# Optimization experiments

Hardware: AMD Instinct MI355X
Metric: run time of the kernel (lower is better)

Reference implementation:

```python
import math
import jax, jax.numpy as jnp
import numpy as np

C_COEF = 3  # module attribute c


def setup_inputs() -> dict:
    key = jax.random.key(0)
    k1, k2, k3 = jax.random.split(key, 3)
    B, L, D = 16, 4096, 64
    return {
        "Q": jax.random.normal(k1, (B, L, D), jnp.float32),
        "K": jax.random.normal(k2, (B, L, D), jnp.float32),
        "V": jax.random.normal(k3, (B, L, D), jnp.float32),
    }


def _fit_len(x, L):
    # K.at[:, 0:L, :].get(mode='fill', fill_value=0): truncate or zero-pad to length L
    S = x.shape[1]
    if S >= L:
        return x[:, :L]
    return jnp.pad(x, ((0, 0), (0, L - S), (0, 0)))


def reference(Q, K, V):
    B, L, D = Q.shape
    K = _fit_len(K, L)
    V = _fit_len(V, L)

    # FFT-based circular cross-correlation Rxx[b, tau, d]
    Qf = jnp.fft.rfft(Q, axis=1)
    Kf = jnpp_rfft = jnp.fft.rfft(K, axis=1)
    Rxx = jnp.fft.irfft(Qf * jnp.conjugate(Kf), n=L, axis=1)  # [B, L, D]

    k = min(int(math.floor(C_COEF * math.log(L))), L)
    # top-k delays per (batch, channel)
    Wk, Ik = jax.lax.top_k(jnp.moveaxis(Rxx, 1, -1), k)  # [B, D, k]
    Wk = jax.nn.softmax(Wk, axis=-1)

    # roll(v, -i)[l] == v[(l + i) % L]  -> single fused gather over all (B, D, k)
    idx = (jnp.arange(L)[None, None, None, :] + Ik[..., None]) % L  # [B, D, k, L]
    Vt = jnp.moveaxis(V, 1, -1)  # [B, D, L]
    Vg = jnp.take_along_axis(Vt[:, :, None, :], idx, axis=3)  # [B, D, k, L]

    # softmax-weighted accumulation over the k delays
    A = jnp.einsum('bdk,bdkl->bld', Wk, Vg)  # [B, L, D]
    return A
```

## Files before the change

kernel.cpp:

```cpp
#include <hip/hip_runtime.h>


#define FFT_N 4096
#define TOPK  24
#define PI2   6.28318530717958647692f
#define C16_1 0.92387953251128675613f
#define S16_1 0.38268343236508977173f
#define C16_2 0.70710678118654752440f

#define V1OFF   4608
#define SM_CAND 36864
#define SM_C0   37376
#define SM_PACK 38400
#define SM_CNT  38608
#define SM_THR  38612
#define SM_SIZE 38624

__device__ __forceinline__ float2 cmul(float2 a, float2 b) {
  return make_float2(a.x*b.x - a.y*b.y, a.x*b.y + a.y*b.x);
}

__device__ __forceinline__ unsigned fkey(float f) {
  int b = __float_as_int(f);
  return (unsigned)(b ^ ((b >> 31) | 0x80000000));
}

template<int S>
__device__ __forceinline__ void fft16(float2* x) {
  const float sg = (float)S;
  float2 y[16];
#pragma unroll
  for (int n2 = 0; n2 < 4; ++n2) {
    float2 a = x[n2], b = x[4+n2], c = x[8+n2], d = x[12+n2];
    float t0r=a.x+c.x, t0i=a.y+c.y, t1r=a.x-c.x, t1i=a.y-c.y;
    float t2r=b.x+d.x, t2i=b.y+d.y, t3r=b.x-d.x, t3i=b.y-d.y;
    y[n2*4+0] = make_float2(t0r+t2r, t0i+t2i);
    y[n2*4+2] = make_float2(t0r-t2r, t0i-t2i);
    y[n2*4+1] = make_float2(t1r - sg*t3i, t1i + sg*t3r);
    y[n2*4+3] = make_float2(t1r + sg*t3i, t1i - sg*t3r);
  }
#define CTW(ii, cc, ss) { float2 v=y[ii]; y[ii]=make_float2(v.x*(cc)-v.y*(sg*(ss)), v.x*(sg*(ss))+v.y*(cc)); }
  CTW(5,  C16_1, S16_1)
  CTW(6,  C16_2, C16_2)
  CTW(7,  S16_1, C16_1)
  CTW(9,  C16_2, C16_2)
  { float2 v = y[10]; y[10] = make_float2(-sg*v.y, sg*v.x); }
  CTW(11, -C16_2, C16_2)
  CTW(13, S16_1, C16_1)
  CTW(14, -C16_2, C16_2)
  CTW(15, -C16_1, -S16_1)
#undef CTW
#pragma unroll
  for (int k1 = 0; k1 < 4; ++k1) {
    float2 a = y[k1], b = y[4+k1], c = y[8+k1], d = y[12+k1];
    float t0r=a.x+c.x, t0i=a.y+c.y, t1r=a.x-c.x, t1i=a.y-c.y;
    float t2r=b.x+d.x, t2i=b.y+d.y, t3r=b.x-d.x, t3i=b.y-d.y;
    x[k1+0]  = make_float2(t0r+t2r, t0i+t2i);
    x[k1+8]  = make_float2(t0r-t2r, t0i-t2i);
    x[k1+4]  = make_float2(t1r - sg*t3i, t1i + sg*t3r);
    x[k1+12] = make_float2(t1r + sg*t3i, t1i - sg*t3r);
  }
}

__device__ __forceinline__ void twiddle_chain(float2* x, float ang) {
  float sb, cb; __sincosf(ang, &sb, &cb);
  float2 w1 = make_float2(cb, sb);
  float2 w2 = cmul(w1,w1), w3 = cmul(w1,w2);
  float2 w4 = cmul(w2,w2), w5 = cmul(w2,w3), w6 = cmul(w3,w3), w7 = cmul(w3,w4);
  float2 w8 = cmul(w4,w4), w9 = cmul(w4,w5), w10 = cmul(w5,w5), w11 = cmul(w5,w6);
  float2 w12 = cmul(w6,w6), w13 = cmul(w6,w7), w14 = cmul(w7,w7), w15 = cmul(w7,w8);
  x[1]=cmul(x[1],w1);   x[2]=cmul(x[2],w2);   x[3]=cmul(x[3],w3);
  x[4]=cmul(x[4],w4);   x[5]=cmul(x[5],w5);   x[6]=cmul(x[6],w6);
  x[7]=cmul(x[7],w7);   x[8]=cmul(x[8],w8);   x[9]=cmul(x[9],w9);
  x[10]=cmul(x[10],w10); x[11]=cmul(x[11],w11); x[12]=cmul(x[12],w12);
  x[13]=cmul(x[13],w13); x[14]=cmul(x[14],w14); x[15]=cmul(x[15],w15);
}

__global__ __launch_bounds__(256) void transposeQKV(const float* __restrict__ Q,
                                                    const float* __restrict__ K,
                                                    const float* __restrict__ V,
                                                    float2* __restrict__ ZQK,
                                                    float* __restrict__ Vt) {
  __shared__ float tq[64][65];
  __shared__ float tk[64][65];
  __shared__ float tv[64][65];
  const int b = blockIdx.y;
  const int t0 = blockIdx.x << 6;
  const float* Qb = Q + ((size_t)b << 18);
  const float* Kb = K + ((size_t)b << 18);
  const float* Vb = V + ((size_t)b << 18);
  int tx = threadIdx.x & 63, ty = threadIdx.x >> 6;
#pragma unroll
  for (int i = 0; i < 16; ++i) {
    int r = (i << 2) + ty;
    tq[r][tx] = Qb[(size_t)(t0 + r) * 64 + tx];
    tk[r][tx] = Kb[(size_t)(t0 + r) * 64 + tx];
    tv[r][tx] = Vb[(size_t)(t0 + r) * 64 + tx];
  }
  __syncthreads();
  float2* zoutb = ZQK + ((size_t)b << 18);
  float*  voutb = Vt + ((size_t)b << 18);
#pragma unroll
  for (int i = 0; i < 16; ++i) {
    int d = (i << 2) + ty;
    zoutb[(size_t)d * 4096 + t0 + tx] = make_float2(tq[tx][d], tk[tx][d]);
    voutb[(size_t)d * 4096 + t0 + tx] = tv[tx][d];
  }
}

__global__ __launch_bounds__(256) void transpose64(const float* __restrict__ in,
                                                   float* __restrict__ out,
                                                   int R, int C) {
  __shared__ float tile[64][65];
  int tiles_c = C >> 6;
  int tr = blockIdx.x / tiles_c;
  int tc = blockIdx.x - tr * tiles_c;
  const float* inb = in + (size_t)blockIdx.y * R * C;
  float* outb = out + (size_t)blockIdx.y * R * C;
  int tx = threadIdx.x & 63;
  int ty = threadIdx.x >> 6;
  int r0 = tr << 6, c0 = tc << 6;
#pragma unroll
  for (int i = 0; i < 16; ++i) {
    int r = (i << 2) + ty;
    tile[r][tx] = inb[(size_t)(r0 + r) * C + (c0 + tx)];
  }
  __syncthreads();
#pragma unroll
  for (int i = 0; i < 16; ++i) {
    int r = (i << 2) + ty;
    outb[(size_t)(c0 + r) * R + (r0 + tx)] = tile[tx][r];
  }
}

__global__ __launch_bounds__(256, 4) void corr_kernel(const float2* __restrict__ ZQK,
                                                      const float* __restrict__ Vt,
                                                      float* __restrict__ At) {
  __shared__ __align__(16) unsigned char smem[SM_SIZE];
  float2* Z = (float2*)smem;

  const int tid = threadIdx.x;
  const size_t row = (size_t)blockIdx.x << 12;

  float2 x[16];

#pragma unroll
  for (int n1 = 0; n1 < 16; ++n1)
    x[n1] = ZQK[row + (n1 << 8) + tid];
  fft16<-1>(x);
  twiddle_chain(x, -PI2 * (float)tid / 4096.f);
#pragma unroll
  for (int k = 0; k < 16; ++k) Z[(k << 8) + tid] = x[k];
  __syncthreads();
  {
    const int k1 = tid >> 4, b = tid & 15;
#pragma unroll
    for (int a = 0; a < 16; ++a) x[a] = Z[(k1 << 8) + (a << 4) + b];
    fft16<-1>(x);
    twiddle_chain(x, -PI2 * (float)b / 256.f);
    __syncthreads();
#pragma unroll
    for (int cc = 0; cc < 16; ++cc) Z[(k1 << 8) + (cc << 4) + (b ^ cc)] = x[cc];
  }
  __syncthreads();
  {
    const int k1 = tid >> 4, c = tid & 15;
#pragma unroll
    for (int bb = 0; bb < 16; ++bb) x[bb] = Z[(k1 << 8) + (c << 4) + (bb ^ c)];
    fft16<-1>(x);
    __syncthreads();
    const int bf = k1 + (c << 4);
#pragma unroll
    for (int d = 0; d < 16; ++d) Z[(bf ^ c) + (d << 8)] = x[d];
  }
  __syncthreads();

  {
    const float scale = 0.25f / 4096.f;
    const int x1 = tid >> 4;
#pragma unroll
    for (int f1 = 0; f1 < 16; ++f1) {
      int f  = (f1 << 8) + tid;
      int fp = (4096 - f) & 4095;
      float2 A  = Z[f ^ x1];
      float2 Bv = Z[fp ^ ((fp >> 4) & 15)];
      float ur = A.x + Bv.x, ui = A.y - Bv.y;
      float vr = A.x - Bv.x, vi = -A.y - Bv.y;
      float xr = ur*vr - ui*vi, xi = ur*vi + ui*vr;
      x[f1] = make_float2(-xi * scale, xr * scale);
    }
  }

  float4 v4s[4];
#pragma unroll
  for (int mm = 0; mm < 4; ++mm)
    v4s[mm] = *(const float4*)&Vt[row + (tid << 2) + (mm << 10)];

  fft16<1>(x);
  twiddle_chain(x, PI2 * (float)tid / 4096.f);
  __syncthreads();
#pragma unroll
  for (int k = 0; k < 16; ++k) Z[(k << 8) + tid] = x[k];
  __syncthreads();
  {
    const int k1 = tid >> 4, b = tid & 15;
#pragma unroll
    for (int a = 0; a < 16; ++a) x[a] = Z[(k1 << 8) + (a << 4) + b];
    fft16<1>(x);
    twiddle_chain(x, PI2 * (float)b / 256.f);
    __syncthreads();
#pragma unroll
    for (int cc = 0; cc < 16; ++cc) Z[(k1 << 8) + (cc << 4) + (b ^ cc)] = x[cc];
  }
  __syncthreads();
  float rr[16];
  {
    const int k1 = tid >> 4, c = tid & 15;
#pragma unroll
    for (int bb = 0; bb < 16; ++bb) x[bb] = Z[(k1 << 8) + (c << 4) + (bb ^ c)];
    fft16<1>(x);
#pragma unroll
    for (int d = 0; d < 16; ++d) rr[d] = x[d].x;
  }
  __syncthreads();

  float* Vf = (float*)smem;
#pragma unroll
  for (int mm = 0; mm < 4; ++mm) {
    int n0 = (tid << 2) + (mm << 10);
    float4 v = v4s[mm];
    *(float4*)&Vf[n0] = v;
    Vf[V1OFF + ((n0 - 1) & 4095)] = v.x;
    Vf[V1OFF + n0]     = v.y;
    Vf[V1OFF + n0 + 1] = v.z;
    Vf[V1OFF + n0 + 2] = v.w;
  }
  {
    float4 v = v4s[0];
    if (tid < 128) {
      *(float4*)&Vf[4096 + (tid << 2)] = v;
      Vf[V1OFF + 4096 + (tid << 2) + 0] = v.y;
      Vf[V1OFF + 4096 + (tid << 2) + 1] = v.z;
      Vf[V1OFF + 4096 + (tid << 2) + 2] = v.w;
    }
    if (tid >= 1 && tid <= 128)
      Vf[V1OFF + 4096 + (tid << 2) - 1] = v.x;
  }
  float c0v = rr[0];
#pragma unroll
  for (int d = 1; d < 16; ++d) c0v = fmaxf(c0v, rr[d]);
  ((float*)(smem + SM_C0))[tid] = c0v;
  if (tid == 0) *(int*)(smem + SM_CNT) = 0;
  __syncthreads();

  if (tid < 64) {
    const float* c0b = (const float*)(smem + SM_C0);
    unsigned k0 = fkey(c0b[tid]);
    unsigned k1 = fkey(c0b[tid + 64]);
    unsigned k2 = fkey(c0b[tid + 128]);
    unsigned k3 = fkey(c0b[tid + 192]);
    unsigned T = 0;
    for (int b = 31; b >= 16; --b) {
      unsigned T2 = T | (1u << b);
      int c = (k0 >= T2) + (k1 >= T2) + (k2 >= T2) + (k3 >= T2);
      unsigned long long b0 = __ballot(c & 1);
      unsigned long long b1 = __ballot(c & 2);
      unsigned long long b2 = __ballot(c & 4);
      int cnt = __popcll(b0) + 2 * __popcll(b1) + 4 * __popcll(b2);
      if (cnt >= TOPK) T = T2;
    }
    if (tid == 0) {
      float thrF;
      if (T == 0) thrF = -3e38f;
      else {
        int ib = (T & 0x80000000u) ? (int)(T ^ 0x80000000u) : (int)~T;
        thrF = __int_as_float(ib);
      }
      *(float*)(smem + SM_THR) = thrF;
    }
  }
  __syncthreads();

  {
    const float thrF = *(const float*)(smem + SM_THR);
    int* cnt = (int*)(smem + SM_CNT);
    float2* cand = (float2*)(smem + SM_CAND);
    const int tb = (tid >> 4) + ((tid & 15) << 4);
#pragma unroll
    for (int d = 0; d < 16; ++d) {
      if (rr[d] >= thrF) {
        int pos = atomicAdd(cnt, 1);
        if (pos < 64)
          cand[pos] = make_float2(rr[d], __int_as_float(tb + (d << 8)));
      }
    }
  }
  __syncthreads();

  if (tid < 64) {
    const float2* cand = (const float2*)(smem + SM_CAND);
    int NC = *(const int*)(smem + SM_CNT);
    NC = NC < 64 ? NC : 64;
    float v; int ix;
    if (tid < NC) { float2 cc = cand[tid]; v = cc.x; ix = __float_as_int(cc.y); }
    else          { v = -3e38f; ix = 0x7fffffff; }
#pragma unroll
    for (int k = 2; k <= 64; k <<= 1) {
#pragma unroll
      for (int j = k >> 1; j > 0; j >>= 1) {
        float ov = __shfl_xor(v, j);
        int   oi = __shfl_xor(ix, j);
        bool iless  = (tid & j) == 0;
        bool dird   = (tid & k) == 0;
        bool better = (v > ov) || (v == ov && ix < oi);
        bool keep   = ((iless == dird) == better);
        v  = keep ? v  : ov;
        ix = keep ? ix : oi;
      }
    }
    float m0 = __shfl(v, 0);
    float e = (tid < TOPK) ? __expf(v - m0) : 0.f;
    float es = e;
#pragma unroll
    for (int off = 32; off; off >>= 1) es += __shfl_xor(es, off);
    float2* pack = (float2*)(smem + SM_PACK);
    if (tid < TOPK) pack[tid] = make_float2(e, __int_as_float(ix));
    if (tid == 0)   pack[TOPK] = make_float2(es, 0.f);
  }
  __syncthreads();

  const float2* pack = (const float2*)(smem + SM_PACK);
  const float inv = 1.0f / pack[TOPK].x;
  float2 a0 = make_float2(0,0), a1=a0, a2=a0, a3=a0, a4=a0, a5=a0, a6=a0, a7=a0;
  const int lbase = tid << 1;
#pragma unroll 1
  for (int t = 0; t < TOPK; ++t) {
    float2 p_ = pack[t];
    float e  = p_.x;
    int   ik = __float_as_int(p_.y);
    int base = ik & ~1;
    const float* Vb = Vf + ((ik & 1) ? V1OFF : 0);
    int e0 = (lbase        + base) & 4095;
    int e1 = (lbase + 1024 + base) & 4095;
    int e2 = (lbase + 2048 + base) & 4095;
    int e3 = (lbase + 3072 + base) & 4095;
    float2 v00 = *(const float2*)&Vb[e0];
    float2 v01 = *(const float2*)&Vb[e0 + 512];
    float2 v10 = *(const float2*)&Vb[e1];
    float2 v11 = *(const float2*)&Vb[e1 + 512];
    float2 v20 = *(const float2*)&Vb[e2];
    float2 v21 = *(const float2*)&Vb[e2 + 512];
    float2 v30 = *(const float2*)&Vb[e3];
    float2 v31 = *(const float2*)&Vb[e3 + 512];
    a0.x += e*v00.x; a0.y += e*v00.y;
    a1.x += e*v01.x; a1.y += e*v01.y;
    a2.x += e*v10.x; a2.y += e*v10.y;
    a3.x += e*v11.x; a3.y += e*v11.y;
    a4.x += e*v20.x; a4.y += e*v20.y;
    a5.x += e*v21.x; a5.y += e*v21.y;
    a6.x += e*v30.x; a6.y += e*v30.y;
    a7.x += e*v31.x; a7.y += e*v31.y;
  }
  *(float2*)&At[row + lbase]        = make_float2(a0.x*inv, a0.y*inv);
  *(float2*)&At[row + lbase + 512]  = make_float2(a1.x*inv, a1.y*inv);
  *(float2*)&At[row + lbase + 1024] = make_float2(a2.x*inv, a2.y*inv);
  *(float2*)&At[row + lbase + 1536] = make_float2(a3.x*inv, a3.y*inv);
  *(float2*)&At[row + lbase + 2048] = make_float2(a4.x*inv, a4.y*inv);
  *(float2*)&At[row + lbase + 2560] = make_float2(a5.x*inv, a5.y*inv);
  *(float2*)&At[row + lbase + 3072] = make_float2(a6.x*inv, a6.y*inv);
  *(float2*)&At[row + lbase + 3584] = make_float2(a7.x*inv, a7.y*inv);
}

extern "C" void kernel_launch(void* const* d_in, const int* in_sizes, int n_in,
                              void* d_out, int out_size, void* d_ws, size_t ws_size,
                              hipStream_t stream) {
  const float* Q = (const float*)d_in[0];
  const float* K = (const float*)d_in[1];
  const float* V = (const float*)d_in[2];
  float* out = (float*)d_out;
  float* wsf = (float*)d_ws;

  const int B = 16;
  const size_t SLAB = (size_t)4194304;
  float2* ZQK = (float2*)wsf;
  float*  Vt  = wsf + 2 * SLAB;
  float*  At  = Vt;

  dim3 blk(256);
  transposeQKV<<<dim3(64, B), blk, 0, stream>>>(Q, K, V, ZQK, Vt);
  corr_kernel<<<dim3(B * 64), blk, 0, stream>>>(ZQK, Vt, At);
  transpose64<<<dim3(64, B), blk, 0, stream>>>(At, out, 64, 4096);
}
```

Baseline: 55.11 us.

## Restructure FFT as radix-8 four-pass with 512 threads per block

Replaces the three-pass radix-16 FFT (256 threads, 16 elements each) with a four-pass radix-8 FFT using 512 threads holding 8 elements each. Padded shared-memory strides (RK1/RK2) are used instead of XOR swizzles in the intermediate passes. The top-k threshold search and the gather/accumulate are adapted to 512 threads, and the output is now written as contiguous float4 chunks. The aim is lower register pressure and more parallelism per block, at the cost of an extra FFT pass and its barriers.

```diff
diff --git a/kernel.cpp b/kernel.cpp
--- a/kernel.cpp
+++ b/kernel.cpp
@@ -1,20 +1,19 @@
 #include <hip/hip_runtime.h>
 
 
-#define FFT_N 4096
 #define TOPK  24
 #define PI2   6.28318530717958647692f
-#define C16_1 0.92387953251128675613f
-#define S16_1 0.38268343236508977173f
-#define C16_2 0.70710678118654752440f
+#define SQH   0.70710678118654752440f
 
 #define V1OFF   4608
-#define SM_CAND 36864
-#define SM_C0   37376
-#define SM_PACK 38400
-#define SM_CNT  38608
-#define SM_THR  38612
-#define SM_SIZE 38624
+#define SM_C0   36864
+#define SM_CAND 38912
+#define SM_PACK 39424
+#define SM_CNT  39624
+#define SM_THR  39628
+#define SM_SIZE 39632
+#define RK1     528
+#define RK2     66
 
 __device__ __forceinline__ float2 cmul(float2 a, float2 b) {
   return make_float2(a.x*b.x - a.y*b.y, a.x*b.y + a.y*b.x);
@@ -25,55 +24,44 @@
   return (unsigned)(b ^ ((b >> 31) | 0x80000000));
 }
 
+__device__ __forceinline__ int SPw(int q) { return q ^ ((q >> 4) & 15); }
+
 template<int S>
-__device__ __forceinline__ void fft16(float2* x) {
+__device__ __forceinline__ void fft8(float2* x) {
   const float sg = (float)S;
-  float2 y[16];
-#pragma unroll
-  for (int n2 = 0; n2 < 4; ++n2) {
-    float2 a = x[n2], b = x[4+n2], c = x[8+n2], d = x[12+n2];
-    float t0r=a.x+c.x, t0i=a.y+c.y, t1r=a.x-c.x, t1i=a.y-c.y;
-    float t2r=b.x+d.x, t2i=b.y+d.y, t3r=b.x-d.x, t3i=b.y-d.y;
-    y[n2*4+0] = make_float2(t0r+t2r, t0i+t2i);
-    y[n2*4+2] = make_float2(t0r-t2r, t0i-t2i);
-    y[n2*4+1] = make_float2(t1r - sg*t3i, t1i + sg*t3r);
-    y[n2*4+3] = make_float2(t1r + sg*t3i, t1i - sg*t3r);
-  }
-#define CTW(ii, cc, ss) { float2 v=y[ii]; y[ii]=make_float2(v.x*(cc)-v.y*(sg*(ss)), v.x*(sg*(ss))+v.y*(cc)); }
-  CTW(5,  C16_1, S16_1)
-  CTW(6,  C16_2, C16_2)
-  CTW(7,  S16_1, C16_1)
-  CTW(9,  C16_2, C16_2)
-  { float2 v = y[10]; y[10] = make_float2(-sg*v.y, sg*v.x); }
-  CTW(11, -C16_2, C16_2)
-  CTW(13, S16_1, C16_1)
-  CTW(14, -C16_2, C16_2)
-  CTW(15, -C16_1, -S16_1)
-#undef CTW
-#pragma unroll
-  for (int k1 = 0; k1 < 4; ++k1) {
-    float2 a = y[k1], b = y[4+k1], c = y[8+k1], d = y[12+k1];
-    float t0r=a.x+c.x, t0i=a.y+c.y, t1r=a.x-c.x, t1i=a.y-c.y;
-    float t2r=b.x+d.x, t2i=b.y+d.y, t3r=b.x-d.x, t3i=b.y-d.y;
-    x[k1+0]  = make_float2(t0r+t2r, t0i+t2i);
-    x[k1+8]  = make_float2(t0r-t2r, t0i-t2i);
-    x[k1+4]  = make_float2(t1r - sg*t3i, t1i + sg*t3r);
-    x[k1+12] = make_float2(t1r + sg*t3i, t1i - sg*t3r);
-  }
-}
-
-__device__ __forceinline__ void twiddle_chain(float2* x, float ang) {
+  float et0r=x[0].x+x[4].x, et0i=x[0].y+x[4].y;
+  float et1r=x[0].x-x[4].x, et1i=x[0].y-x[4].y;
+  float et2r=x[2].x+x[6].x, et2i=x[2].y+x[6].y;
+  float et3r=x[2].x-x[6].x, et3i=x[2].y-x[6].y;
+  float E0r=et0r+et2r, E0i=et0i+et2i;
+  float E2r=et0r-et2r, E2i=et0i-et2i;
+  float E1r=et1r-sg*et3i, E1i=et1i+sg*et3r;
+  float E3r=et1r+sg*et3i, E3i=et1i-sg*et3r;
+  float ot0r=x[1].x+x[5].x, ot0i=x[1].y+x[5].y;
+  float ot1r=x[1].x-x[5].x, ot1i=x[1].y-x[5].y;
+  float ot2r=x[3].x+x[7].x, ot2i=x[3].y+x[7].y;
+  float ot3r=x[3].x-x[7].x, ot3i=x[3].y-x[7].y;
+  float O0r=ot0r+ot2r, O0i=ot0i+ot2i;
+  float O2r=ot0r-ot2r, O2i=ot0i-ot2i;
+  float O1r=ot1r-sg*ot3i, O1i=ot1i+sg*ot3r;
+  float O3r=ot1r+sg*ot3i, O3i=ot1i-sg*ot3r;
+  float T1r = SQH*(O1r - sg*O1i), T1i = SQH*(O1i + sg*O1r);
+  float T2r = -sg*O2i,            T2i = sg*O2r;
+  float T3r = -SQH*(O3r + sg*O3i), T3i = SQH*(sg*O3r - O3i);
+  x[0]=make_float2(E0r+O0r, E0i+O0i);  x[4]=make_float2(E0r-O0r, E0i-O0i);
+  x[1]=make_float2(E1r+T1r, E1i+T1i);  x[5]=make_float2(E1r-T1r, E1i-T1i);
+  x[2]=make_float2(E2r+T2r, E2i+T2i);  x[6]=make_float2(E2r-T2r, E2i-T2i);
+  x[3]=make_float2(E3r+T3r, E3i+T3i);  x[7]=make_float2(E3r-T3r, E3i-T3i);
+}
+
+__device__ __forceinline__ void twiddle8(float2* x, float ang) {
   float sb, cb; __sincosf(ang, &sb, &cb);
   float2 w1 = make_float2(cb, sb);
-  float2 w2 = cmul(w1,w1), w3 = cmul(w1,w2);
-  float2 w4 = cmul(w2,w2), w5 = cmul(w2,w3), w6 = cmul(w3,w3), w7 = cmul(w3,w4);
-  float2 w8 = cmul(w4,w4), w9 = cmul(w4,w5), w10 = cmul(w5,w5), w11 = cmul(w5,w6);
-  float2 w12 = cmul(w6,w6), w13 = cmul(w6,w7), w14 = cmul(w7,w7), w15 = cmul(w7,w8);
-  x[1]=cmul(x[1],w1);   x[2]=cmul(x[2],w2);   x[3]=cmul(x[3],w3);
-  x[4]=cmul(x[4],w4);   x[5]=cmul(x[5],w5);   x[6]=cmul(x[6],w6);
-  x[7]=cmul(x[7],w7);   x[8]=cmul(x[8],w8);   x[9]=cmul(x[9],w9);
-  x[10]=cmul(x[10],w10); x[11]=cmul(x[11],w11); x[12]=cmul(x[12],w12);
-  x[13]=cmul(x[13],w13); x[14]=cmul(x[14],w14); x[15]=cmul(x[15],w15);
+  float2 w2 = cmul(w1,w1), w3 = cmul(w2,w1);
+  float2 w4 = cmul(w2,w2), w5 = cmul(w3,w2), w6 = cmul(w3,w3), w7 = cmul(w4,w3);
+  x[1]=cmul(x[1],w1); x[2]=cmul(x[2],w2); x[3]=cmul(x[3],w3);
+  x[4]=cmul(x[4],w4); x[5]=cmul(x[5],w5); x[6]=cmul(x[6],w6);
+  x[7]=cmul(x[7],w7);
 }
 
 __global__ __launch_bounds__(256) void transposeQKV(const float* __restrict__ Q,
@@ -133,101 +121,133 @@
   }
 }
 
-__global__ __launch_bounds__(256, 4) void corr_kernel(const float2* __restrict__ ZQK,
+__global__ __launch_bounds__(512, 8) void corr_kernel(const float2* __restrict__ ZQK,
                                                       const float* __restrict__ Vt,
                                                       float* __restrict__ At) {
   __shared__ __align__(16) unsigned char smem[SM_SIZE];
   float2* Z = (float2*)smem;
 
   const int tid = threadIdx.x;
+  const int k1 = tid >> 6;
   const size_t row = (size_t)blockIdx.x << 12;
 
-  float2 x[16];
-
-#pragma unroll
-  for (int n1 = 0; n1 < 16; ++n1)
-    x[n1] = ZQK[row + (n1 << 8) + tid];
-  fft16<-1>(x);
-  twiddle_chain(x, -PI2 * (float)tid / 4096.f);
-#pragma unroll
-  for (int k = 0; k < 16; ++k) Z[(k << 8) + tid] = x[k];
-  __syncthreads();
-  {
-    const int k1 = tid >> 4, b = tid & 15;
-#pragma unroll
-    for (int a = 0; a < 16; ++a) x[a] = Z[(k1 << 8) + (a << 4) + b];
-    fft16<-1>(x);
-    twiddle_chain(x, -PI2 * (float)b / 256.f);
-    __syncthreads();
-#pragma unroll
-    for (int cc = 0; cc < 16; ++cc) Z[(k1 << 8) + (cc << 4) + (b ^ cc)] = x[cc];
-  }
-  __syncthreads();
-  {
-    const int k1 = tid >> 4, c = tid & 15;
-#pragma unroll
-    for (int bb = 0; bb < 16; ++bb) x[bb] = Z[(k1 << 8) + (c << 4) + (bb ^ c)];
-    fft16<-1>(x);
-    __syncthreads();
-    const int bf = k1 + (c << 4);
-#pragma unroll
-    for (int d = 0; d < 16; ++d) Z[(bf ^ c) + (d << 8)] = x[d];
+  float2 x[8];
+
+#pragma unroll
+  for (int j = 0; j < 8; ++j)
+    x[j] = ZQK[row + (j << 9) + tid];
+  fft8<-1>(x);
+  twiddle8(x, -PI2 * (float)tid / 4096.f);
+#pragma unroll
+  for (int k = 0; k < 8; ++k) Z[k * RK1 + tid] = x[k];
+  __syncthreads();
+
+  {
+    const int u = tid & 63;
+    float2* Zb = Z + k1 * RK1;
+#pragma unroll
+    for (int a = 0; a < 8; ++a) x[a] = Zb[(a << 6) + u];
+    fft8<-1>(x);
+    twiddle8(x, -PI2 * (float)u / 512.f);
+    __syncthreads();
+#pragma unroll
+    for (int k = 0; k < 8; ++k) Zb[k * RK2 + u] = x[k];
+  }
+  __syncthreads();
+
+  {
+    const int k2 = (tid >> 3) & 7, v = tid & 7;
+    float2* Zb = Z + k1 * RK1 + k2 * RK2;
+#pragma unroll
+    for (int b = 0; b < 8; ++b) x[b] = Zb[(b << 3) + v];
+    fft8<-1>(x);
+    twiddle8(x, -PI2 * (float)v / 64.f);
+    __syncthreads();
+#pragma unroll
+    for (int k = 0; k < 8; ++k) Zb[(k << 3) + v] = x[k];
+  }
+  __syncthreads();
+
+  const int flo = k1 + (((tid >> 3) & 7) << 3) + ((tid & 7) << 6);
+  {
+    const int k2 = (tid >> 3) & 7, k3 = tid & 7;
+    const float2* Zb = Z + k1 * RK1 + k2 * RK2 + (k3 << 3);
+#pragma unroll
+    for (int c = 0; c < 8; ++c) x[c] = Zb[c];
+    fft8<-1>(x);
+    __syncthreads();
+#pragma unroll
+    for (int d = 0; d < 8; ++d) Z[SPw(flo + (d << 9))] = x[d];
   }
   __syncthreads();
 
   {
     const float scale = 0.25f / 4096.f;
-    const int x1 = tid >> 4;
-#pragma unroll
-    for (int f1 = 0; f1 < 16; ++f1) {
-      int f  = (f1 << 8) + tid;
+    const int sw_own = (tid >> 4) & 15;
+#pragma unroll
+    for (int j = 0; j < 8; ++j) {
+      int f  = (j << 9) + tid;
       int fp = (4096 - f) & 4095;
-      float2 A  = Z[f ^ x1];
-      float2 Bv = Z[fp ^ ((fp >> 4) & 15)];
+      float2 A  = Z[f ^ sw_own];
+      float2 Bv = Z[SPw(fp)];
       float ur = A.x + Bv.x, ui = A.y - Bv.y;
       float vr = A.x - Bv.x, vi = -A.y - Bv.y;
       float xr = ur*vr - ui*vi, xi = ur*vi + ui*vr;
-      x[f1] = make_float2(-xi * scale, xr * scale);
-    }
-  }
-
-  float4 v4s[4];
-#pragma unroll
-  for (int mm = 0; mm < 4; ++mm)
-    v4s[mm] = *(const float4*)&Vt[row + (tid << 2) + (mm << 10)];
-
-  fft16<1>(x);
-  twiddle_chain(x, PI2 * (float)tid / 4096.f);
-  __syncthreads();
-#pragma unroll
-  for (int k = 0; k < 16; ++k) Z[(k << 8) + tid] = x[k];
-  __syncthreads();
-  {
-    const int k1 = tid >> 4, b = tid & 15;
-#pragma unroll
-    for (int a = 0; a < 16; ++a) x[a] = Z[(k1 << 8) + (a << 4) + b];
-    fft16<1>(x);
-    twiddle_chain(x, PI2 * (float)b / 256.f);
-    __syncthreads();
-#pragma unroll
-    for (int cc = 0; cc < 16; ++cc) Z[(k1 << 8) + (cc << 4) + (b ^ cc)] = x[cc];
-  }
-  __syncthreads();
-  float rr[16];
-  {
-    const int k1 = tid >> 4, c = tid & 15;
-#pragma unroll
-    for (int bb = 0; bb < 16; ++bb) x[bb] = Z[(k1 << 8) + (c << 4) + (bb ^ c)];
-    fft16<1>(x);
-#pragma unroll
-    for (int d = 0; d < 16; ++d) rr[d] = x[d].x;
+      x[j] = make_float2(-xi * scale, xr * scale);
+    }
+  }
+
+  float4 v4s[2];
+#pragma unroll
+  for (int mm = 0; mm < 2; ++mm)
+    v4s[mm] = *(const float4*)&Vt[row + (tid << 2) + (mm << 11)];
+  __syncthreads();
+
+  fft8<1>(x);
+  twiddle8(x, PI2 * (float)tid / 4096.f);
+#pragma unroll
+  for (int k = 0; k < 8; ++k) Z[k * RK1 + tid] = x[k];
+  __syncthreads();
+  {
+    const int u = tid & 63;
+    float2* Zb = Z + k1 * RK1;
+#pragma unroll
+    for (int a = 0; a < 8; ++a) x[a] = Zb[(a << 6) + u];
+    fft8<1>(x);
+    twiddle8(x, PI2 * (float)u / 512.f);
+    __syncthreads();
+#pragma unroll
+    for (int k = 0; k < 8; ++k) Zb[k * RK2 + u] = x[k];
+  }
+  __syncthreads();
+  {
+    const int k2 = (tid >> 3) & 7, v = tid & 7;
+    float2* Zb = Z + k1 * RK1 + k2 * RK2;
+#pragma unroll
+    for (int b = 0; b < 8; ++b) x[b] = Zb[(b << 3) + v];
+    fft8<1>(x);
+    twiddle8(x, PI2 * (float)v / 64.f);
+    __syncthreads();
+#pragma unroll
+    for (int k = 0; k < 8; ++k) Zb[(k << 3) + v] = x[k];
+  }
+  __syncthreads();
+  float rr[8];
+  {
+    const int k2 = (tid >> 3) & 7, k3 = tid & 7;
+    const float2* Zb = Z + k1 * RK1 + k2 * RK2 + (k3 << 3);
+#pragma unroll
+    for (int c = 0; c < 8; ++c) x[c] = Zb[c];
+    fft8<1>(x);
+#pragma unroll
+    for (int d = 0; d < 8; ++d) rr[d] = x[d].x;
   }
   __syncthreads();
 
   float* Vf = (float*)smem;
 #pragma unroll
-  for (int mm = 0; mm < 4; ++mm) {
-    int n0 = (tid << 2) + (mm << 10);
+  for (int mm = 0; mm < 2; ++mm) {
+    int n0 = (tid << 2) + (mm << 11);
     float4 v = v4s[mm];
     *(float4*)&Vf[n0] = v;
     Vf[V1OFF + ((n0 - 1) & 4095)] = v.x;
@@ -248,25 +268,27 @@
   }
   float c0v = rr[0];
 #pragma unroll
-  for (int d = 1; d < 16; ++d) c0v = fmaxf(c0v, rr[d]);
+  for (int d = 1; d < 8; ++d) c0v = fmaxf(c0v, rr[d]);
   ((float*)(smem + SM_C0))[tid] = c0v;
   if (tid == 0) *(int*)(smem + SM_CNT) = 0;
   __syncthreads();
 
   if (tid < 64) {
     const float* c0b = (const float*)(smem + SM_C0);
-    unsigned k0 = fkey(c0b[tid]);
-    unsigned k1 = fkey(c0b[tid + 64]);
-    unsigned k2 = fkey(c0b[tid + 128]);
-    unsigned k3 = fkey(c0b[tid + 192]);
+    unsigned kk[8];
+#pragma unroll
+    for (int m = 0; m < 8; ++m) kk[m] = fkey(c0b[tid + (m << 6)]);
     unsigned T = 0;
     for (int b = 31; b >= 16; --b) {
       unsigned T2 = T | (1u << b);
-      int c = (k0 >= T2) + (k1 >= T2) + (k2 >= T2) + (k3 >= T2);
+      int c = 0;
+#pragma unroll
+      for (int m = 0; m < 8; ++m) c += (kk[m] >= T2) ? 1 : 0;
       unsigned long long b0 = __ballot(c & 1);
       unsigned long long b1 = __ballot(c & 2);
       unsigned long long b2 = __ballot(c & 4);
-      int cnt = __popcll(b0) + 2 * __popcll(b1) + 4 * __popcll(b2);
+      unsigned long long b3 = __ballot(c & 8);
+      int cnt = __popcll(b0) + 2*__popcll(b1) + 4*__popcll(b2) + 8*__popcll(b3);
       if (cnt >= TOPK) T = T2;
     }
     if (tid == 0) {
@@ -285,13 +307,12 @@
     const float thrF = *(const float*)(smem + SM_THR);
     int* cnt = (int*)(smem + SM_CNT);
     float2* cand = (float2*)(smem + SM_CAND);
-    const int tb = (tid >> 4) + ((tid & 15) << 4);
-#pragma unroll
-    for (int d = 0; d < 16; ++d) {
+#pragma unroll
+    for (int d = 0; d < 8; ++d) {
       if (rr[d] >= thrF) {
         int pos = atomicAdd(cnt, 1);
         if (pos < 64)
-          cand[pos] = make_float2(rr[d], __int_as_float(tb + (d << 8)));
+          cand[pos] = make_float2(rr[d], __int_as_float(flo + (d << 9)));
       }
     }
   }
@@ -331,8 +352,8 @@
 
   const float2* pack = (const float2*)(smem + SM_PACK);
   const float inv = 1.0f / pack[TOPK].x;
-  float2 a0 = make_float2(0,0), a1=a0, a2=a0, a3=a0, a4=a0, a5=a0, a6=a0, a7=a0;
-  const int lbase = tid << 1;
+  float2 a0 = make_float2(0,0), a1 = a0, a2 = a0, a3 = a0;
+  const int o = tid << 3;
 #pragma unroll 1
   for (int t = 0; t < TOPK; ++t) {
     float2 p_ = pack[t];
@@ -340,35 +361,20 @@
     int   ik = __float_as_int(p_.y);
     int base = ik & ~1;
     const float* Vb = Vf + ((ik & 1) ? V1OFF : 0);
-    int e0 = (lbase        + base) & 4095;
-    int e1 = (lbase + 1024 + base) & 4095;
-    int e2 = (lbase + 2048 + base) & 4095;
-    int e3 = (lbase + 3072 + base) & 4095;
-    float2 v00 = *(const float2*)&Vb[e0];
-    float2 v01 = *(const float2*)&Vb[e0 + 512];
-    float2 v10 = *(const float2*)&Vb[e1];
-    float2 v11 = *(const float2*)&Vb[e1 + 512];
-    float2 v20 = *(const float2*)&Vb[e2];
-    float2 v21 = *(const float2*)&Vb[e2 + 512];
-    float2 v30 = *(const float2*)&Vb[e3];
-    float2 v31 = *(const float2*)&Vb[e3 + 512];
-    a0.x += e*v00.x; a0.y += e*v00.y;
-    a1.x += e*v01.x; a1.y += e*v01.y;
-    a2.x += e*v10.x; a2.y += e*v10.y;
-    a3.x += e*v11.x; a3.y += e*v11.y;
-    a4.x += e*v20.x; a4.y += e*v20.y;
-    a5.x += e*v21.x; a5.y += e*v21.y;
-    a6.x += e*v30.x; a6.y += e*v30.y;
-    a7.x += e*v31.x; a7.y += e*v31.y;
-  }
-  *(float2*)&At[row + lbase]        = make_float2(a0.x*inv, a0.y*inv);
-  *(float2*)&At[row + lbase + 512]  = make_float2(a1.x*inv, a1.y*inv);
-  *(float2*)&At[row + lbase + 1024] = make_float2(a2.x*inv, a2.y*inv);
-  *(float2*)&At[row + lbase + 1536] = make_float2(a3.x*inv, a3.y*inv);
-  *(float2*)&At[row + lbase + 2048] = make_float2(a4.x*inv, a4.y*inv);
-  *(float2*)&At[row + lbase + 2560] = make_float2(a5.x*inv, a5.y*inv);
-  *(float2*)&At[row + lbase + 3072] = make_float2(a6.x*inv, a6.y*inv);
-  *(float2*)&At[row + lbase + 3584] = make_float2(a7.x*inv, a7.y*inv);
+    int e0 = (o + base) & 4095;
+    float2 v0 = *(const float2*)&Vb[e0];
+    float2 v1 = *(const float2*)&Vb[e0 + 2];
+    float2 v2 = *(const float2*)&Vb[e0 + 4];
+    float2 v3 = *(const float2*)&Vb[e0 + 6];
+    a0.x += e*v0.x; a0.y += e*v0.y;
+    a1.x += e*v1.x; a1.y += e*v1.y;
+    a2.x += e*v2.x; a2.y += e*v2.y;
+    a3.x += e*v3.x; a3.y += e*v3.y;
+  }
+  float4 r0 = make_float4(a0.x*inv, a0.y*inv, a1.x*inv, a1.y*inv);
+  float4 r1 = make_float4(a2.x*inv, a2.y*inv, a3.x*inv, a3.y*inv);
+  *(float4*)&At[row + o]     = r0;
+  *(float4*)&At[row + o + 4] = r1;
 }
 
 extern "C" void kernel_launch(void* const* d_in, const int* in_sizes, int n_in,
@@ -388,6 +394,6 @@
 
   dim3 blk(256);
   transposeQKV<<<dim3(64, B), blk, 0, stream>>>(Q, K, V, ZQK, Vt);
-  corr_kernel<<<dim3(B * 64), blk, 0, stream>>>(ZQK, Vt, At);
+  corr_kernel<<<dim3(B * 64), dim3(512), 0, stream>>>(ZQK, Vt, At);
   transpose64<<<dim3(64, B), blk, 0, stream>>>(At, out, 64, 4096);
 }
```

After: 70.00 us. +27.0%, slower.

## Pad FFT shared rows and drop barriers between warp-local FFT stages

Applied to the files above, without the earlier changes.

Shared-memory rows in the first FFT stage are padded to a stride of 272, so the column-wise reads no longer conflict. The second and third radix-16 stages now exchange data through a 16-thread private region without a block barrier, which removes several __syncthreads calls per FFT. The shifted copy of V is rebuilt with wrap-around indexing instead of extended buffers, which shrinks shared memory use. The risk is that the barrier-free exchange relies on the 16 threads of a group sitting in the same wavefront, and the shifted copy adds an extra barrier plus reads from shared memory.

```diff
diff --git a/kernel.cpp b/kernel.cpp
--- a/kernel.cpp
+++ b/kernel.cpp
@@ -1,20 +1,20 @@
 #include <hip/hip_runtime.h>
 
 
-#define FFT_N 4096
 #define TOPK  24
 #define PI2   6.28318530717958647692f
 #define C16_1 0.92387953251128675613f
 #define S16_1 0.38268343236508977173f
 #define C16_2 0.70710678118654752440f
 
-#define V1OFF   4608
-#define SM_CAND 36864
-#define SM_C0   37376
-#define SM_PACK 38400
-#define SM_CNT  38608
-#define SM_THR  38612
-#define SM_SIZE 38624
+#define RK    272
+#define V1OFF   4096
+#define SM_C0   34816
+#define SM_CAND 35840
+#define SM_PACK 36352
+#define SM_CNT  36552
+#define SM_THR  36556
+#define SM_SIZE 36560
 
 __device__ __forceinline__ float2 cmul(float2 a, float2 b) {
   return make_float2(a.x*b.x - a.y*b.y, a.x*b.y + a.y*b.x);
@@ -140,6 +140,7 @@
   float2* Z = (float2*)smem;
 
   const int tid = threadIdx.x;
+  const int k1 = tid >> 4, bq = tid & 15;
   const size_t row = (size_t)blockIdx.x << 12;
 
   float2 x[16];
@@ -150,39 +151,35 @@
   fft16<-1>(x);
   twiddle_chain(x, -PI2 * (float)tid / 4096.f);
 #pragma unroll
-  for (int k = 0; k < 16; ++k) Z[(k << 8) + tid] = x[k];
-  __syncthreads();
-  {
-    const int k1 = tid >> 4, b = tid & 15;
-#pragma unroll
-    for (int a = 0; a < 16; ++a) x[a] = Z[(k1 << 8) + (a << 4) + b];
+  for (int k = 0; k < 16; ++k) Z[k * RK + tid] = x[k];
+  __syncthreads();
+
+  {
+#pragma unroll
+    for (int a = 0; a < 16; ++a) x[a] = Z[k1 * RK + (a << 4) + bq];
     fft16<-1>(x);
-    twiddle_chain(x, -PI2 * (float)b / 256.f);
-    __syncthreads();
-#pragma unroll
-    for (int cc = 0; cc < 16; ++cc) Z[(k1 << 8) + (cc << 4) + (b ^ cc)] = x[cc];
-  }
-  __syncthreads();
-  {
-    const int k1 = tid >> 4, c = tid & 15;
-#pragma unroll
-    for (int bb = 0; bb < 16; ++bb) x[bb] = Z[(k1 << 8) + (c << 4) + (bb ^ c)];
+    twiddle_chain(x, -PI2 * (float)bq / 256.f);
+#pragma unroll
+    for (int cc = 0; cc < 16; ++cc) Z[k1 * RK + (cc << 4) + (bq ^ cc)] = x[cc];
+#pragma unroll
+    for (int bb = 0; bb < 16; ++bb) x[bb] = Z[k1 * RK + (bq << 4) + (bb ^ bq)];
     fft16<-1>(x);
-    __syncthreads();
-    const int bf = k1 + (c << 4);
-#pragma unroll
-    for (int d = 0; d < 16; ++d) Z[(bf ^ c) + (d << 8)] = x[d];
+  }
+  __syncthreads();
+  {
+    const int bf = k1 + (bq << 4);
+#pragma unroll
+    for (int d = 0; d < 16; ++d) Z[(bf ^ bq) + (d << 8)] = x[d];
   }
   __syncthreads();
 
   {
     const float scale = 0.25f / 4096.f;
-    const int x1 = tid >> 4;
 #pragma unroll
     for (int f1 = 0; f1 < 16; ++f1) {
       int f  = (f1 << 8) + tid;
       int fp = (4096 - f) & 4095;
-      float2 A  = Z[f ^ x1];
+      float2 A  = Z[f ^ k1];
       float2 Bv = Z[fp ^ ((fp >> 4) & 15)];
       float ur = A.x + Bv.x, ui = A.y - Bv.y;
       float vr = A.x - Bv.x, vi = -A.y - Bv.y;
@@ -195,74 +192,58 @@
 #pragma unroll
   for (int mm = 0; mm < 4; ++mm)
     v4s[mm] = *(const float4*)&Vt[row + (tid << 2) + (mm << 10)];
+  __syncthreads();
 
   fft16<1>(x);
   twiddle_chain(x, PI2 * (float)tid / 4096.f);
-  __syncthreads();
-#pragma unroll
-  for (int k = 0; k < 16; ++k) Z[(k << 8) + tid] = x[k];
-  __syncthreads();
-  {
-    const int k1 = tid >> 4, b = tid & 15;
-#pragma unroll
-    for (int a = 0; a < 16; ++a) x[a] = Z[(k1 << 8) + (a << 4) + b];
+#pragma unroll
+  for (int k = 0; k < 16; ++k) Z[k * RK + tid] = x[k];
+  __syncthreads();
+  {
+#pragma unroll
+    for (int a = 0; a < 16; ++a) x[a] = Z[k1 * RK + (a << 4) + bq];
     fft16<1>(x);
-    twiddle_chain(x, PI2 * (float)b / 256.f);
-    __syncthreads();
-#pragma unroll
-    for (int cc = 0; cc < 16; ++cc) Z[(k1 << 8) + (cc << 4) + (b ^ cc)] = x[cc];
-  }
-  __syncthreads();
+    twiddle_chain(x, PI2 * (float)bq / 256.f);
+#pragma unroll
+    for (int cc = 0; cc < 16; ++cc) Z[k1 * RK + (cc << 4) + (bq ^ cc)] = x[cc];
+#pragma unroll
+    for (int bb = 0; bb < 16; ++bb) x[bb] = Z[k1 * RK + (bq << 4) + (bb ^ bq)];
+    fft16<1>(x);
+  }
   float rr[16];
-  {
-    const int k1 = tid >> 4, c = tid & 15;
-#pragma unroll
-    for (int bb = 0; bb < 16; ++bb) x[bb] = Z[(k1 << 8) + (c << 4) + (bb ^ c)];
-    fft16<1>(x);
-#pragma unroll
-    for (int d = 0; d < 16; ++d) rr[d] = x[d].x;
-  }
+#pragma unroll
+  for (int d = 0; d < 16; ++d) rr[d] = x[d].x;
   __syncthreads();
 
   float* Vf = (float*)smem;
+#pragma unroll
+  for (int mm = 0; mm < 4; ++mm)
+    *(float4*)&Vf[(tid << 2) + (mm << 10)] = v4s[mm];
+  float c0v = rr[0];
+#pragma unroll
+  for (int d = 1; d < 16; ++d) c0v = fmaxf(c0v, rr[d]);
+  ((float*)(smem + SM_C0))[tid] = c0v;
+  if (tid == 0) *(int*)(smem + SM_CNT) = 0;
+  __syncthreads();
+
 #pragma unroll
   for (int mm = 0; mm < 4; ++mm) {
     int n0 = (tid << 2) + (mm << 10);
     float4 v = v4s[mm];
-    *(float4*)&Vf[n0] = v;
-    Vf[V1OFF + ((n0 - 1) & 4095)] = v.x;
-    Vf[V1OFF + n0]     = v.y;
-    Vf[V1OFF + n0 + 1] = v.z;
-    Vf[V1OFF + n0 + 2] = v.w;
-  }
-  {
-    float4 v = v4s[0];
-    if (tid < 128) {
-      *(float4*)&Vf[4096 + (tid << 2)] = v;
-      Vf[V1OFF + 4096 + (tid << 2) + 0] = v.y;
-      Vf[V1OFF + 4096 + (tid << 2) + 1] = v.z;
-      Vf[V1OFF + 4096 + (tid << 2) + 2] = v.w;
-    }
-    if (tid >= 1 && tid <= 128)
-      Vf[V1OFF + 4096 + (tid << 2) - 1] = v.x;
-  }
-  float c0v = rr[0];
-#pragma unroll
-  for (int d = 1; d < 16; ++d) c0v = fmaxf(c0v, rr[d]);
-  ((float*)(smem + SM_C0))[tid] = c0v;
-  if (tid == 0) *(int*)(smem + SM_CNT) = 0;
-  __syncthreads();
+    float nx = Vf[(n0 + 4) & 4095];
+    *(float4*)&Vf[V1OFF + n0] = make_float4(v.y, v.z, v.w, nx);
+  }
 
   if (tid < 64) {
     const float* c0b = (const float*)(smem + SM_C0);
-    unsigned k0 = fkey(c0b[tid]);
-    unsigned k1 = fkey(c0b[tid + 64]);
-    unsigned k2 = fkey(c0b[tid + 128]);
-    unsigned k3 = fkey(c0b[tid + 192]);
+    unsigned kk0 = fkey(c0b[tid]);
+    unsigned kk1 = fkey(c0b[tid + 64]);
+    unsigned kk2 = fkey(c0b[tid + 128]);
+    unsigned kk3 = fkey(c0b[tid + 192]);
     unsigned T = 0;
     for (int b = 31; b >= 16; --b) {
       unsigned T2 = T | (1u << b);
-      int c = (k0 >= T2) + (k1 >= T2) + (k2 >= T2) + (k3 >= T2);
+      int c = (kk0 >= T2) + (kk1 >= T2) + (kk2 >= T2) + (kk3 >= T2);
       unsigned long long b0 = __ballot(c & 1);
       unsigned long long b1 = __ballot(c & 2);
       unsigned long long b2 = __ballot(c & 4);
@@ -285,7 +266,7 @@
     const float thrF = *(const float*)(smem + SM_THR);
     int* cnt = (int*)(smem + SM_CNT);
     float2* cand = (float2*)(smem + SM_CAND);
-    const int tb = (tid >> 4) + ((tid & 15) << 4);
+    const int tb = k1 + (bq << 4);
 #pragma unroll
     for (int d = 0; d < 16; ++d) {
       if (rr[d] >= thrF) {
@@ -332,7 +313,7 @@
   const float2* pack = (const float2*)(smem + SM_PACK);
   const float inv = 1.0f / pack[TOPK].x;
   float2 a0 = make_float2(0,0), a1=a0, a2=a0, a3=a0, a4=a0, a5=a0, a6=a0, a7=a0;
-  const int lbase = tid << 1;
+  const int o2 = tid << 1;
 #pragma unroll 1
   for (int t = 0; t < TOPK; ++t) {
     float2 p_ = pack[t];
@@ -340,35 +321,18 @@
     int   ik = __float_as_int(p_.y);
     int base = ik & ~1;
     const float* Vb = Vf + ((ik & 1) ? V1OFF : 0);
-    int e0 = (lbase        + base) & 4095;
-    int e1 = (lbase + 1024 + base) & 4095;
-    int e2 = (lbase + 2048 + base) & 4095;
-    int e3 = (lbase + 3072 + base) & 4095;
-    float2 v00 = *(const float2*)&Vb[e0];
-    float2 v01 = *(const float2*)&Vb[e0 + 512];
-    float2 v10 = *(const float2*)&Vb[e1];
-    float2 v11 = *(const float2*)&Vb[e1 + 512];
-    float2 v20 = *(const float2*)&Vb[e2];
-    float2 v21 = *(const float2*)&Vb[e2 + 512];
-    float2 v30 = *(const float2*)&Vb[e3];
-    float2 v31 = *(const float2*)&Vb[e3 + 512];
-    a0.x += e*v00.x; a0.y += e*v00.y;
-    a1.x += e*v01.x; a1.y += e*v01.y;
-    a2.x += e*v10.x; a2.y += e*v10.y;
-    a3.x += e*v11.x; a3.y += e*v11.y;
-    a4.x += e*v20.x; a4.y += e*v20.y;
-    a5.x += e*v21.x; a5.y += e*v21.y;
-    a6.x += e*v30.x; a6.y += e*v30.y;
-    a7.x += e*v31.x; a7.y += e*v31.y;
-  }
-  *(float2*)&At[row + lbase]        = make_float2(a0.x*inv, a0.y*inv);
-  *(float2*)&At[row + lbase + 512]  = make_float2(a1.x*inv, a1.y*inv);
-  *(float2*)&At[row + lbase + 1024] = make_float2(a2.x*inv, a2.y*inv);
-  *(float2*)&At[row + lbase + 1536] = make_float2(a3.x*inv, a3.y*inv);
-  *(float2*)&At[row + lbase + 2048] = make_float2(a4.x*inv, a4.y*inv);
-  *(float2*)&At[row + lbase + 2560] = make_float2(a5.x*inv, a5.y*inv);
-  *(float2*)&At[row + lbase + 3072] = make_float2(a6.x*inv, a6.y*inv);
-  *(float2*)&At[row + lbase + 3584] = make_float2(a7.x*inv, a7.y*inv);
+#define GSTEP(acc, MM) { int e0 = (o2 + (MM << 9) + base) & 4095;             \
+    float2 vv = *(const float2*)&Vb[e0];                                      \
+    acc.x += e * vv.x; acc.y += e * vv.y; }
+    GSTEP(a0, 0) GSTEP(a1, 1) GSTEP(a2, 2) GSTEP(a3, 3)
+    GSTEP(a4, 4) GSTEP(a5, 5) GSTEP(a6, 6) GSTEP(a7, 7)
+#undef GSTEP
+  }
+#define WSTEP(acc, MM) { *(float2*)&At[row + o2 + (MM << 9)] =                \
+    make_float2(acc.x * inv, acc.y * inv); }
+  WSTEP(a0, 0) WSTEP(a1, 1) WSTEP(a2, 2) WSTEP(a3, 3)
+  WSTEP(a4, 4) WSTEP(a5, 5) WSTEP(a6, 6) WSTEP(a7, 7)
+#undef WSTEP
 }
 
 extern "C" void kernel_launch(void* const* d_in, const int* in_sizes, int n_in,
```

Result: slower. 57.74 us (+4.8%).
